# Performance work log

Hardware: AMD Instinct MI355X
Metric: run time of the kernel (lower is better)

The kernel has to match this reference:

```python
import jax, jax.numpy as jnp
import numpy as np

BN_EPS = 1e-5
N_SH, N_SS, N_HH, D = 1195, 390, 805, 64


def _gcn(x, edge_index, W, b, n_nodes, mean):
    # per-edge message = Linear(x_j); lin(x)[src] == lin(x[src])
    h = x @ W + b                                   # [N, out]
    msg = h[edge_index[0]]                          # gather sources -> [E, out]
    agg = jax.ops.segment_sum(msg, edge_index[1], num_segments=n_nodes)
    if mean:
        cnt = jax.ops.segment_sum(jnp.ones((edge_index.shape[1],), x.dtype),
                                  edge_index[1], num_segments=n_nodes)
        agg = agg / jnp.maximum(cnt, 1.0)[:, None]
    return jnp.tanh(agg)


def _bn(x, gamma, beta):
    # BatchNorm1d in training mode: biased batch statistics
    m = jnp.mean(x, axis=0)
    v = jnp.var(x, axis=0)
    return (x - m) * jax.lax.rsqrt(v + BN_EPS) * gamma + beta


def setup_inputs() -> dict:
    key = jax.random.key(0)
    ks = jax.random.split(key, 40)
    f32 = jnp.float32

    def lin(k, din, dout):
        k1, k2 = jax.random.split(k)
        s = 1.0 / np.sqrt(din)
        W = jax.random.uniform(k1, (din, dout), f32, -s, s)
        b = jax.random.uniform(k2, (dout,), f32, -s, s)
        return W, b

    inp = {}
    inp["x_SH"] = jnp.arange(N_SH, dtype=jnp.int64 if jax.config.jax_enable_x64 else jnp.int32)
    inp["edge_index_SH"] = jax.random.randint(ks[0], (2, 1_000_000), 0, N_SH)
    inp["x_SS"] = jnp.arange(N_SS)
    inp["edge_index_SS"] = jax.random.randint(ks[1], (2, 200_000), 0, N_SS)
    inp["x_HH"] = jnp.arange(N_HH)
    inp["edge_index_HH"] = jax.random.randint(ks[2], (2, 200_000), 0, N_HH)
    inp["prescription"] = jax.random.uniform(ks[3], (20000, N_SS), f32)
    inp["kgOneHot"] = jax.random.uniform(ks[4], (N_HH, 27), f32)

    inp["emb"] = jax.random.normal(ks[5], (N_SH, D), f32)
    inp["w_sh1"], inp["b_sh1"] = lin(ks[6], D, D)
    inp["w_sh2"], inp["b_sh2"] = lin(ks[7], D, D)
    inp["w_mlp1"], inp["b_mlp1"] = lin(ks[8], D, 256)
    inp["g_bn1"] = jnp.ones((256,), f32); inp["be_bn1"] = jnp.zeros((256,), f32)
    inp["w_sh1h"], inp["b_sh1h"] = lin(ks[9], D, D)
    inp["w_sh2h"], inp["b_sh2h"] = lin(ks[10], D, D)
    inp["w_mlp1h"], inp["b_mlp1h"] = lin(ks[11], D, 256)
    inp["g_bn1h"] = jnp.ones((256,), f32); inp["be_bn1h"] = jnp.zeros((256,), f32)
    inp["w_ss"], inp["b_ss"] = lin(ks[12], D, 256)
    inp["w_hh"], inp["b_hh"] = lin(ks[13], D + 27, 256)
    inp["w_mlp"], inp["b_mlp"] = lin(ks[14], 256, 256)
    inp["g_si"] = jnp.ones((256,), f32); inp["be_si"] = jnp.zeros((256,), f32)
    return inp


def reference(x_SH, edge_index_SH, x_SS, edge_index_SS, x_HH, edge_index_HH,
              prescription, kgOneHot, emb,
              w_sh1, b_sh1, w_sh2, b_sh2, w_mlp1, b_mlp1, g_bn1, be_bn1,
              w_sh1h, b_sh1h, w_sh2h, b_sh2h, w_mlp1h, b_mlp1h, g_bn1h, be_bn1h,
              w_ss, b_ss, w_hh, b_hh, w_mlp, b_mlp, g_si, be_si):
    # symptom branch on SH graph (mean aggregation)
    x1 = emb[x_SH]                                           # [1195, 64]
    x2 = _gcn(x1, edge_index_SH, w_sh1, b_sh1, N_SH, mean=True)
    x6 = _gcn(x2, edge_index_SH, w_sh2, b_sh2, N_SH, mean=True)
    x9 = (x1 + x2 + x6) / 3.0
    x9 = jnp.tanh(_bn(x9 @ w_mlp1 + b_mlp1, g_bn1, be_bn1))  # [1195, 256]

    # herb branch on SH graph
    x22 = _gcn(x1, edge_index_SH, w_sh1h, b_sh1h, N_SH, mean=True)
    x66 = _gcn(x22, edge_index_SH, w_sh2h, b_sh2h, N_SH, mean=True)
    x99 = (x1 + x22 + x66) / 3.0
    x99 = jnp.tanh(_bn(x99 @ w_mlp1h + b_mlp1h, g_bn1h, be_bn1h))

    # SS graph (add aggregation)
    x_ss1 = _gcn(emb[x_SS], edge_index_SS, w_ss, b_ss, N_SS, mean=False)  # [390, 256]

    # HH graph with KG one-hot features appended
    x_hh0 = jnp.concatenate([emb[x_HH], kgOneHot], axis=-1)  # [805, 91]
    x_hh1 = _gcn(x_hh0, edge_index_HH, w_hh, b_hh, N_HH, mean=False)      # [805, 256]

    es = x9[:N_SS] + x_ss1                                   # [390, 256]
    eh = x99[N_SS:] + x_hh1                                  # [805, 256]

    e_synd = prescription @ es                               # [B, 256]
    pre_sum = jnp.sum(prescription, axis=1, keepdims=True)
    e = e_synd / pre_sum
    e = jax.nn.relu(_bn(e @ w_mlp + b_mlp, g_si, be_si))
    return e @ eh.T                                          # [B, 805]
```

## Files before the change

### kernel.cpp

```cpp
#include <hip/hip_runtime.h>
#include <cstddef>
#include <cstdint>

#define N_SH 1195
#define N_SS 390
#define N_HH 805
#define DIM  64

typedef __bf16 bf16_t;
typedef bf16_t bf16x4v __attribute__((ext_vector_type(4)));
typedef bf16_t bf16x8v __attribute__((ext_vector_type(8)));
typedef float f32x4 __attribute__((ext_vector_type(4)));

__device__ inline ushort f2bf(float f) {
    union { float f; uint32_t u; } c; c.f = f;
    uint32_t u = c.u;
    u += 0x7FFFu + ((u >> 16) & 1u);
    return (ushort)(u >> 16);
}

__device__ inline void xcd_swizzle(int gx, int gy, int& bx, int& by) {
    int nwg = gx * gy;
    int lin = by * gx + bx;
    int q = nwg >> 3, r = nwg & 7;
    int xcd = lin & 7, idx = lin >> 3;
    int nt = (xcd < r ? xcd * (q + 1) : r * (q + 1) + (xcd - r) * q) + idx;
    by = nt / gx; bx = nt % gx;
}

__global__ void build_adj_packed_kernel(const int* __restrict__ ei, int E,
                                        int halfStride, uint32_t* __restrict__ T) {
    int i = blockIdx.x * blockDim.x + threadIdx.x;
    if (i < E) {
        int src = ei[i];
        int dst = ei[E + i];
        atomicAdd(&T[(size_t)dst * halfStride + (src >> 1)], 1u << ((src & 1) * 16));
    }
}

__global__ void rowsum_inv_packed_kernel(const uint32_t* __restrict__ T, int R,
                                         int halfStride, float* __restrict__ inv) {
    int row  = blockIdx.x * (blockDim.x / 64) + (threadIdx.x / 64);
    int lane = threadIdx.x & 63;
    if (row >= R) return;
    const uint32_t* p = T + (size_t)row * halfStride;
    uint32_t s = 0;
    for (int c = lane; c < halfStride; c += 64) {
        uint32_t w = p[c];
        s += (w & 0xFFFFu) + (w >> 16);
    }
    for (int off = 32; off > 0; off >>= 1) s += __shfl_down(s, off);
    if (lane == 0) inv[row] = 1.0f / fmaxf((float)s, 1.0f);
}

__global__ void cvt_unpack_kernel(const uint32_t* __restrict__ T, int R, int C,
                                  int halfStride, ushort* __restrict__ out,
                                  int Rp, int Cp) {
    int i = blockIdx.x * blockDim.x + threadIdx.x;
    if (i >= Rp * Cp) return;
    int r = i / Cp, c = i % Cp;
    float v = 0.f;
    if (r < R && c < C) {
        uint32_t w = T[(size_t)r * halfStride + (c >> 1)];
        v = (float)((w >> ((c & 1) * 16)) & 0xFFFFu);
    }
    out[i] = f2bf(v);
}

#define BM 64
#define BN 64
#define BK 16

__global__ __launch_bounds__(256) void gemm_kernel(
    const float* __restrict__ A, const float* __restrict__ B,
    const float* __restrict__ bias, const float* __restrict__ rowScale,
    float* __restrict__ C, int M, int N, int K, int act)
{
    __shared__ float As[BK][BM + 4];
    __shared__ float Bs[BK][BN];
    const int tid  = threadIdx.x;
    const int row0 = blockIdx.y * BM;
    const int col0 = blockIdx.x * BN;
    const int tr  = (tid >> 4) << 2;
    const int tc  = (tid & 15) << 2;
    const int lar = tid >> 2;
    const int lac = (tid & 3) << 2;
    const int lbr = tid >> 4;
    const int lbc = (tid & 15) << 2;

    float acc[4][4] = {{0.f}};

    for (int k0 = 0; k0 < K; k0 += BK) {
        const int gr = row0 + lar;
        const float* Ap = A + (size_t)gr * K + k0 + lac;
        #pragma unroll
        for (int i = 0; i < 4; ++i) {
            int gk = k0 + lac + i;
            As[lac + i][lar] = (gr < M && gk < K) ? Ap[i] : 0.f;
        }
        const int gk = k0 + lbr;
        const float* Bp = B + (size_t)gk * N + col0 + lbc;
        #pragma unroll
        for (int i = 0; i < 4; ++i) {
            int gc = col0 + lbc + i;
            Bs[lbr][lbc + i] = (gk < K && gc < N) ? Bp[i] : 0.f;
        }
        __syncthreads();
        #pragma unroll
        for (int kk = 0; kk < BK; ++kk) {
            float4 a = *reinterpret_cast<const float4*>(&As[kk][tr]);
            float4 b = *reinterpret_cast<const float4*>(&Bs[kk][tc]);
            acc[0][0] += a.x * b.x; acc[0][1] += a.x * b.y; acc[0][2] += a.x * b.z; acc[0][3] += a.x * b.w;
            acc[1][0] += a.y * b.x; acc[1][1] += a.y * b.y; acc[1][2] += a.y * b.z; acc[1][3] += a.y * b.w;
            acc[2][0] += a.z * b.x; acc[2][1] += a.z * b.y; acc[2][2] += a.z * b.z; acc[2][3] += a.z * b.w;
            acc[3][0] += a.w * b.x; acc[3][1] += a.w * b.y; acc[3][2] += a.w * b.z; acc[3][3] += a.w * b.w;
        }
        __syncthreads();
    }

    #pragma unroll
    for (int i = 0; i < 4; ++i) {
        int gr = row0 + tr + i;
        if (gr >= M) continue;
        float rs = rowScale ? rowScale[gr] : 1.0f;
        #pragma unroll
        for (int j = 0; j < 4; ++j) {
            int gc = col0 + tc + j;
            if (gc >= N) continue;
            float v = acc[i][j];
            if (bias) v += bias[gc];
            v *= rs;
            if (act == 1) v = tanhf(v);
            C[(size_t)gr * N + gc] = v;
        }
    }
}

#define LDT 40

__global__ __launch_bounds__(256) void mfma_gemm_kernel(
    const ushort* __restrict__ A, const ushort* __restrict__ Bt,
    int M, int Nw, int K, int lda,
    const float* __restrict__ bias, const float* __restrict__ rowScale,
    float* __restrict__ outF, ushort* __restrict__ outB, ushort* __restrict__ outLo,
    int ldo, float* __restrict__ statsOut)
{
    __shared__ __align__(16) ushort As[128 * LDT];
    __shared__ __align__(16) ushort Bs[128 * LDT];
    __shared__ float cs[256];
    const int tid  = threadIdx.x;
    int bx = blockIdx.x, by = blockIdx.y;
    xcd_swizzle(gridDim.x, gridDim.y, bx, by);
    const int row0 = by * 128;
    const int col0 = bx * 128;
    const int wid  = tid >> 6, lane = tid & 63;
    const int wr = wid >> 1, wc = wid & 1;
    const int l15 = lane & 15, lg = lane >> 4;
    const int kg = lg * 4;
    const int sr = tid >> 2;
    const int sc = (tid & 3) * 8;

    const ushort* pA0 = A  + (size_t)(row0 + sr)      * lda + sc;
    const ushort* pA1 = A  + (size_t)(row0 + sr + 64) * lda + sc;
    const ushort* pB0 = Bt + (size_t)(col0 + sr)      * lda + sc;
    const ushort* pB1 = Bt + (size_t)(col0 + sr + 64) * lda + sc;

    uint4 ra0 = *reinterpret_cast<const uint4*>(pA0);
    uint4 ra1 = *reinterpret_cast<const uint4*>(pA1);
    uint4 rb0 = *reinterpret_cast<const uint4*>(pB0);
    uint4 rb1 = *reinterpret_cast<const uint4*>(pB1);

    f32x4 acc[4][4];
    #pragma unroll
    for (int m = 0; m < 4; ++m)
        #pragma unroll
        for (int n = 0; n < 4; ++n) acc[m][n] = (f32x4)0.f;

    for (int k0 = 0; k0 < K; k0 += 32) {
        *reinterpret_cast<uint4*>(&As[sr * LDT + sc])        = ra0;
        *reinterpret_cast<uint4*>(&As[(sr + 64) * LDT + sc]) = ra1;
        *reinterpret_cast<uint4*>(&Bs[sr * LDT + sc])        = rb0;
        *reinterpret_cast<uint4*>(&Bs[(sr + 64) * LDT + sc]) = rb1;
        __syncthreads();
        if (k0 + 32 < K) {
            ra0 = *reinterpret_cast<const uint4*>(pA0 + k0 + 32);
            ra1 = *reinterpret_cast<const uint4*>(pA1 + k0 + 32);
            rb0 = *reinterpret_cast<const uint4*>(pB0 + k0 + 32);
            rb1 = *reinterpret_cast<const uint4*>(pB1 + k0 + 32);
        }

        bf16x8v af[4], bfr[4];
        #pragma unroll
        for (int m = 0; m < 4; ++m) {
            int ar = wr * 64 + m * 16 + l15;
            bf16x4v lo = *reinterpret_cast<const bf16x4v*>(&As[ar * LDT + kg]);
            bf16x4v hi = *reinterpret_cast<const bf16x4v*>(&As[ar * LDT + kg + 16]);
            af[m] = __builtin_shufflevector(lo, hi, 0, 1, 2, 3, 4, 5, 6, 7);
        }
        #pragma unroll
        for (int n = 0; n < 4; ++n) {
            int br = wc * 64 + n * 16 + l15;
            bf16x4v lo = *reinterpret_cast<const bf16x4v*>(&Bs[br * LDT + kg]);
            bf16x4v hi = *reinterpret_cast<const bf16x4v*>(&Bs[br * LDT + kg + 16]);
            bfr[n] = __builtin_shufflevector(lo, hi, 0, 1, 2, 3, 4, 5, 6, 7);
        }
        #pragma unroll
        for (int m = 0; m < 4; ++m)
            #pragma unroll
            for (int n = 0; n < 4; ++n)
                acc[m][n] = __builtin_amdgcn_mfma_f32_16x16x32_bf16(af[m], bfr[n], acc[m][n], 0, 0, 0);
        __syncthreads();
    }

    float ls[4] = {0.f, 0.f, 0.f, 0.f}, lq[4] = {0.f, 0.f, 0.f, 0.f};
    #pragma unroll
    for (int m = 0; m < 4; ++m) {
        int grow_base = row0 + wr * 64 + m * 16 + kg;
        #pragma unroll
        for (int j = 0; j < 4; ++j) {
            int grow = grow_base + j;
            if (grow >= M) continue;
            float rs = rowScale ? rowScale[grow] : 1.0f;
            #pragma unroll
            for (int n = 0; n < 4; ++n) {
                int gcol = col0 + wc * 64 + n * 16 + l15;
                if (gcol >= Nw) continue;
                float v = acc[m][n][j];
                if (bias) v += bias[gcol];
                v *= rs;
                if (outB) {
                    ushort h = f2bf(v);
                    outB[(size_t)grow * ldo + gcol] = h;
                    if (outLo) {
                        float hv = __uint_as_float(((uint32_t)h) << 16);
                        outLo[(size_t)grow * ldo + gcol] = f2bf(v - hv);
                    }
                } else {
                    outF[(size_t)grow * ldo + gcol] = v;
                    ls[n] += v; lq[n] += v * v;
                }
            }
        }
    }

    if (statsOut) {
        if (tid < 256) cs[tid] = 0.f;
        __syncthreads();
        #pragma unroll
        for (int n = 0; n < 4; ++n) {
            int lc = wc * 64 + n * 16 + l15;
            atomicAdd(&cs[lc], ls[n]);
            atomicAdd(&cs[128 + lc], lq[n]);
        }
        __syncthreads();
        if (tid < 128) {
            atomicAdd(&statsOut[col0 + tid], cs[tid]);
            atomicAdd(&statsOut[256 + col0 + tid], cs[128 + tid]);
        }
    }
}

__device__ inline void loadP8(const float* __restrict__ rowp, int c0, bool rv,
                              float* a, float& s) {
    if (rv && c0 + 8 <= N_SS) {
        float2 x0 = *reinterpret_cast<const float2*>(rowp + c0);
        float2 x1 = *reinterpret_cast<const float2*>(rowp + c0 + 2);
        float2 x2 = *reinterpret_cast<const float2*>(rowp + c0 + 4);
        float2 x3 = *reinterpret_cast<const float2*>(rowp + c0 + 6);
        a[0] = x0.x; a[1] = x0.y; a[2] = x1.x; a[3] = x1.y;
        a[4] = x2.x; a[5] = x2.y; a[6] = x3.x; a[7] = x3.y;
    } else {
        #pragma unroll
        for (int i = 0; i < 8; ++i) a[i] = (rv && (c0 + i) < N_SS) ? rowp[c0 + i] : 0.f;
    }
    #pragma unroll
    for (int i = 0; i < 8; ++i) s += a[i];
}

__global__ __launch_bounds__(256) void mfma_c1_kernel(
    const float* __restrict__ Pm, const ushort* __restrict__ Bt,
    int M, ushort* __restrict__ outB, ushort* __restrict__ outLo, int ldo)
{
    __shared__ __align__(16) ushort As[128 * LDT];
    __shared__ __align__(16) ushort Bs[128 * LDT];
    __shared__ float sums[128];
    const int tid  = threadIdx.x;
// ... 155 lines not shown
            *reinterpret_cast<uint4*>(&As[sr * LDT + sc]) = *reinterpret_cast<const uint4*>(h);
            h[0] = (bf16_t)fmaxf(a10.x * s8[0] + t8[0], 0.f);
            h[1] = (bf16_t)fmaxf(a10.y * s8[1] + t8[1], 0.f);
            h[2] = (bf16_t)fmaxf(a10.z * s8[2] + t8[2], 0.f);
            h[3] = (bf16_t)fmaxf(a10.w * s8[3] + t8[3], 0.f);
            h[4] = (bf16_t)fmaxf(a11.x * s8[4] + t8[4], 0.f);
            h[5] = (bf16_t)fmaxf(a11.y * s8[5] + t8[5], 0.f);
            h[6] = (bf16_t)fmaxf(a11.z * s8[6] + t8[6], 0.f);
            h[7] = (bf16_t)fmaxf(a11.w * s8[7] + t8[7], 0.f);
            *reinterpret_cast<uint4*>(&As[(sr + 64) * LDT + sc]) = *reinterpret_cast<const uint4*>(h);
        }
        *reinterpret_cast<uint4*>(&Bs[sr * LDT + sc])        = b0;
        *reinterpret_cast<uint4*>(&Bs[(sr + 64) * LDT + sc]) = b1;
        __syncthreads();
        if (k0 + 32 < 256) {
            a00 = *reinterpret_cast<const float4*>(pA0 + k0 + 32);
            a01 = *reinterpret_cast<const float4*>(pA0 + k0 + 36);
            a10 = *reinterpret_cast<const float4*>(pA1 + k0 + 32);
            a11 = *reinterpret_cast<const float4*>(pA1 + k0 + 36);
            b0  = *reinterpret_cast<const uint4*>(pB0 + k0 + 32);
            b1  = *reinterpret_cast<const uint4*>(pB1 + k0 + 32);
        }

        bf16x8v af[4], bfr[4];
        #pragma unroll
        for (int m = 0; m < 4; ++m) {
            int ar = wr * 64 + m * 16 + l15;
            bf16x4v lo = *reinterpret_cast<const bf16x4v*>(&As[ar * LDT + kg]);
            bf16x4v hi = *reinterpret_cast<const bf16x4v*>(&As[ar * LDT + kg + 16]);
            af[m] = __builtin_shufflevector(lo, hi, 0, 1, 2, 3, 4, 5, 6, 7);
        }
        #pragma unroll
        for (int n = 0; n < 4; ++n) {
            int br = wc * 64 + n * 16 + l15;
            bf16x4v lo = *reinterpret_cast<const bf16x4v*>(&Bs[br * LDT + kg]);
            bf16x4v hi = *reinterpret_cast<const bf16x4v*>(&Bs[br * LDT + kg + 16]);
            bfr[n] = __builtin_shufflevector(lo, hi, 0, 1, 2, 3, 4, 5, 6, 7);
        }
        #pragma unroll
        for (int m = 0; m < 4; ++m)
            #pragma unroll
            for (int n = 0; n < 4; ++n)
                acc[m][n] = __builtin_amdgcn_mfma_f32_16x16x32_bf16(af[m], bfr[n], acc[m][n], 0, 0, 0);
        __syncthreads();
    }

    #pragma unroll
    for (int m = 0; m < 4; ++m) {
        int grow_base = row0 + wr * 64 + m * 16 + kg;
        #pragma unroll
        for (int j = 0; j < 4; ++j) {
            int grow = grow_base + j;
            if (grow >= M) continue;
            #pragma unroll
            for (int n = 0; n < 4; ++n) {
                int gcol = col0 + wc * 64 + n * 16 + l15;
                if (gcol >= Nw) continue;
                outF[(size_t)grow * ldo + gcol] = acc[m][n][j];
            }
        }
    }
}

__global__ __launch_bounds__(256) void mfma_splitk_kernel(
    const ushort* __restrict__ A, const ushort* __restrict__ Bt,
    int M, int K, int lda, int kChunk, int Ntot,
    float* __restrict__ part)
{
    __shared__ __align__(16) ushort As[128 * LDT];
    __shared__ __align__(16) ushort Bs[128 * LDT];
    const int tid  = threadIdx.x;
    const int row0 = blockIdx.y * 128;
    const int col0 = blockIdx.x * 128;
    const int wid  = tid >> 6, lane = tid & 63;
    const int wr = wid >> 1, wc = wid & 1;
    const int l15 = lane & 15, lg = lane >> 4;
    const int kg = lg * 4;
    const int sr = tid >> 2;
    const int sc = (tid & 3) * 8;

    const int k0s = blockIdx.z * kChunk;
    const int k0e = (k0s + kChunk < K) ? k0s + kChunk : K;

    const ushort* pA0 = A  + (size_t)(row0 + sr)      * lda + sc;
    const ushort* pA1 = A  + (size_t)(row0 + sr + 64) * lda + sc;
    const ushort* pB0 = Bt + (size_t)(col0 + sr)      * lda + sc;
    const ushort* pB1 = Bt + (size_t)(col0 + sr + 64) * lda + sc;

    uint4 ra0 = *reinterpret_cast<const uint4*>(pA0 + k0s);
    uint4 ra1 = *reinterpret_cast<const uint4*>(pA1 + k0s);
    uint4 rb0 = *reinterpret_cast<const uint4*>(pB0 + k0s);
    uint4 rb1 = *reinterpret_cast<const uint4*>(pB1 + k0s);

    f32x4 acc[4][4];
    #pragma unroll
    for (int m = 0; m < 4; ++m)
        #pragma unroll
        for (int n = 0; n < 4; ++n) acc[m][n] = (f32x4)0.f;

    for (int k0 = k0s; k0 < k0e; k0 += 32) {
        *reinterpret_cast<uint4*>(&As[sr * LDT + sc])        = ra0;
        *reinterpret_cast<uint4*>(&As[(sr + 64) * LDT + sc]) = ra1;
        *reinterpret_cast<uint4*>(&Bs[sr * LDT + sc])        = rb0;
        *reinterpret_cast<uint4*>(&Bs[(sr + 64) * LDT + sc]) = rb1;
        __syncthreads();
        if (k0 + 32 < k0e) {
            ra0 = *reinterpret_cast<const uint4*>(pA0 + k0 + 32);
            ra1 = *reinterpret_cast<const uint4*>(pA1 + k0 + 32);
            rb0 = *reinterpret_cast<const uint4*>(pB0 + k0 + 32);
            rb1 = *reinterpret_cast<const uint4*>(pB1 + k0 + 32);
        }

        bf16x8v af[4], bfr[4];
        #pragma unroll
        for (int m = 0; m < 4; ++m) {
            int ar = wr * 64 + m * 16 + l15;
            bf16x4v lo = *reinterpret_cast<const bf16x4v*>(&As[ar * LDT + kg]);
            bf16x4v hi = *reinterpret_cast<const bf16x4v*>(&As[ar * LDT + kg + 16]);
            af[m] = __builtin_shufflevector(lo, hi, 0, 1, 2, 3, 4, 5, 6, 7);
        }
        #pragma unroll
        for (int n = 0; n < 4; ++n) {
            int br = wc * 64 + n * 16 + l15;
            bf16x4v lo = *reinterpret_cast<const bf16x4v*>(&Bs[br * LDT + kg]);
            bf16x4v hi = *reinterpret_cast<const bf16x4v*>(&Bs[br * LDT + kg + 16]);
            bfr[n] = __builtin_shufflevector(lo, hi, 0, 1, 2, 3, 4, 5, 6, 7);
        }
        #pragma unroll
        for (int m = 0; m < 4; ++m)
            #pragma unroll
            for (int n = 0; n < 4; ++n)
                acc[m][n] = __builtin_amdgcn_mfma_f32_16x16x32_bf16(af[m], bfr[n], acc[m][n], 0, 0, 0);
        __syncthreads();
    }

    float* pslab = part + (size_t)blockIdx.z * M * Ntot;
    #pragma unroll
    for (int m = 0; m < 4; ++m) {
        int grow_base = row0 + wr * 64 + m * 16 + kg;
        #pragma unroll
        for (int j = 0; j < 4; ++j) {
            int grow = grow_base + j;
            if (grow >= M) continue;
            #pragma unroll
            for (int n = 0; n < 4; ++n) {
                int gcol = col0 + wc * 64 + n * 16 + l15;
                pslab[(size_t)grow * Ntot + gcol] = acc[m][n][j];
            }
        }
    }
}

__global__ void reduce_tanh_kernel(const float* __restrict__ part, int S, int M, int N,
                                   const float* __restrict__ rs, float* __restrict__ out) {
    int i = blockIdx.x * blockDim.x + threadIdx.x;
    if (i >= M * N) return;
    int r = i / N;
    float s = 0.f;
    for (int z = 0; z < S; ++z) s += part[(size_t)z * M * N + i];
    if (rs) s *= rs[r];
    out[i] = tanhf(s);
}

__global__ void transpose_cvt_kernel(const float* __restrict__ in, int K, int N, int ldin,
                                     ushort* __restrict__ out, int Kp) {
    int i = blockIdx.x * blockDim.x + threadIdx.x;
    if (i >= N * Kp) return;
    int n = i / Kp, k = i % Kp;
    float v = (k < K) ? in[(size_t)k * ldin + n] : 0.f;
    out[i] = f2bf(v);
}

__global__ void make_cat_weights_kernel(
    const float* __restrict__ w_sh1, const float* __restrict__ w_sh1h,
    const float* __restrict__ b_sh1, const float* __restrict__ b_sh1h,
    const float* __restrict__ w_sh2, const float* __restrict__ w_sh2h,
    const float* __restrict__ b_sh2, const float* __restrict__ b_sh2h,
    const float* __restrict__ w_mlp1, const float* __restrict__ w_mlp1h,
    const float* __restrict__ b_mlp1, const float* __restrict__ b_mlp1h,
    float* __restrict__ W1cat, float* __restrict__ b1cat,
    float* __restrict__ W2bd,  float* __restrict__ b2cat,
    float* __restrict__ WMbd,  float* __restrict__ bMcat)
{
    int i = blockIdx.x * blockDim.x + threadIdx.x;
    if (i < 64 * 128) {
        int k = i >> 7, j = i & 127;
        W1cat[i] = (j < 64) ? w_sh1[k * 64 + j] : w_sh1h[k * 64 + (j - 64)];
        return;
    }
    i -= 64 * 128;
    if (i < 128) { b1cat[i] = (i < 64) ? b_sh1[i] : b_sh1h[i - 64]; return; }
    i -= 128;
    if (i < 128 * 128) {
        int k = i >> 7, j = i & 127;
        float v = 0.f;
        if (k < 64 && j < 64) v = w_sh2[k * 64 + j];
        else if (k >= 64 && j >= 64) v = w_sh2h[(k - 64) * 64 + (j - 64)];
        W2bd[i] = v;
        return;
    }
    i -= 128 * 128;
    if (i < 128) { b2cat[i] = (i < 64) ? b_sh2[i] : b_sh2h[i - 64]; return; }
    i -= 128;
    if (i < 128 * 512) {
        int k = i >> 9, j = i & 511;
        float v = 0.f;
        if (j < 256) { if (k < 64) v = w_mlp1[k * 256 + j]; }
        else         { if (k >= 64) v = w_mlp1h[(k - 64) * 256 + (j - 256)]; }
        WMbd[i] = v;
        return;
    }
    i -= 128 * 512;
    if (i < 512) { bMcat[i] = (i < 256) ? b_mlp1[i] : b_mlp1h[i - 256]; }
}

__global__ void avg3cat_kernel(const float* __restrict__ emb, const float* __restrict__ x2cat,
                               const float* __restrict__ x6cat, float* __restrict__ o) {
    int i = blockIdx.x * blockDim.x + threadIdx.x;
    if (i >= N_SH * 128) return;
    int r = i >> 7, j = i & 127;
    o[i] = (emb[r * 64 + (j & 63)] + x2cat[i] + x6cat[i]) * (1.0f / 3.0f);
}

__global__ void concat_hh_kernel(const float* __restrict__ emb, const float* __restrict__ kg,
                                 float* __restrict__ out) {
    int i = blockIdx.x * blockDim.x + threadIdx.x;
    const int n = N_HH * 91;
    if (i >= n) return;
    int r = i / 91, c = i % 91;
    out[i] = (c < DIM) ? emb[r * DIM + c] : kg[r * 27 + (c - DIM)];
}

__global__ void make_esbt_kernel(const float* __restrict__ x9cat, const float* __restrict__ ss1,
                                 ushort* __restrict__ out, int Kp) {
    int i = blockIdx.x * blockDim.x + threadIdx.x;
    if (i >= 256 * Kp) return;
    int n = i / Kp, k = i % Kp;
    float v = (k < N_SS) ? (x9cat[(size_t)k * 512 + n] + ss1[(size_t)k * 256 + n]) : 0.f;
    out[i] = f2bf(v);
}

__global__ void make_wmlp2_kernel(const float* __restrict__ wm, ushort* __restrict__ out) {
    int i = blockIdx.x * blockDim.x + threadIdx.x;
    if (i >= 256 * 512) return;
    int n = i >> 9, k = i & 511;
    out[i] = f2bf(wm[(size_t)(k & 255) * 256 + n]);
}

__global__ void make_ehb_kernel(const float* __restrict__ x9cat, const float* __restrict__ hh1,
                                ushort* __restrict__ out, int Rp) {
    int i = blockIdx.x * blockDim.x + threadIdx.x;
    if (i >= Rp * 256) return;
    int r = i >> 8, c = i & 255;
    float v = (r < N_HH) ? (x9cat[(size_t)(N_SS + r) * 512 + 256 + c] + hh1[(size_t)r * 256 + c]) : 0.f;
    out[i] = f2bf(v);
}

__global__ void bn_stats_cat_kernel(const float* __restrict__ X, int M,
                                    float* __restrict__ stats) {
    int j = threadIdx.x;
    float s = 0.f, ss = 0.f;
    for (int r = blockIdx.x; r < M; r += gridDim.x) {
        float v = X[(size_t)r * 512 + j];
        s += v; ss += v * v;
    }
    atomicAdd(&stats[j], s);
    atomicAdd(&stats[512 + j], ss);
}

__global__ void bn_apply_cat_kernel(const float* __restrict__ X, const float* __restrict__ stats,
                                    const float* __restrict__ g1, const float* __restrict__ be1,
                                    const float* __restrict__ g2, const float* __restrict__ be2,
                                    int M, float* __restrict__ out) {
    int i = blockIdx.x * blockDim.x + threadIdx.x;
    if (i >= M * 512) return;
    int j = i & 511;
    float invM = 1.0f / (float)M;
    float mean = stats[j] * invM;
    float var  = fmaxf(stats[512 + j] * invM - mean * mean, 0.f);
    float ga = (j < 256) ? g1[j]  : g2[j - 256];
    float bb = (j < 256) ? be1[j] : be2[j - 256];
    float y = (X[i] - mean) * rsqrtf(var + 1e-5f) * ga + bb;
    out[i] = tanhf(y);
}

__global__ void bn_finalize_kernel(const float* __restrict__ stats,
                                   const float* __restrict__ g, const float* __restrict__ be,
                                   int M, float* __restrict__ scale, float* __restrict__ shift) {
    int j = threadIdx.x;
    float invM = 1.0f / (float)M;
    float mean = stats[j] * invM;
    float var  = fmaxf(stats[256 + j] * invM - mean * mean, 0.f);
    float sc = g[j] * rsqrtf(var + 1e-5f);
    scale[j] = sc;
    shift[j] = be[j] - mean * sc;
}

extern "C" void kernel_launch(void* const* d_in, const int* in_sizes, int n_in,
                              void* d_out, int out_size, void* d_ws, size_t ws_size,
                              hipStream_t stream) {
    const int*   eiSH = (const int*)d_in[1];
    const int*   eiSS = (const int*)d_in[3];
    const int*   eiHH = (const int*)d_in[5];
    const float* P    = (const float*)d_in[6];
    const float* kg   = (const float*)d_in[7];
    const float* emb  = (const float*)d_in[8];
    const float* w_sh1  = (const float*)d_in[9];   const float* b_sh1  = (const float*)d_in[10];
    const float* w_sh2  = (const float*)d_in[11];  const float* b_sh2  = (const float*)d_in[12];
    const float* w_mlp1 = (const float*)d_in[13];  const float* b_mlp1 = (const float*)d_in[14];
    const float* g_bn1  = (const float*)d_in[15];  const float* be_bn1 = (const float*)d_in[16];
    const float* w_sh1h = (const float*)d_in[17];  const float* b_sh1h = (const float*)d_in[18];
    const float* w_sh2h = (const float*)d_in[19];  const float* b_sh2h = (const float*)d_in[20];
    const float* w_mlp1h= (const float*)d_in[21];  const float* b_mlp1h= (const float*)d_in[22];
    const float* g_bn1h = (const float*)d_in[23];  const float* be_bn1h= (const float*)d_in[24];
    const float* w_ss   = (const float*)d_in[25];  const float* b_ss   = (const float*)d_in[26];
    const float* w_hh   = (const float*)d_in[27];  const float* b_hh   = (const float*)d_in[28];
    const float* w_mlp  = (const float*)d_in[29];  const float* b_mlp  = (const float*)d_in[30];
    const float* g_si   = (const float*)d_in[31];  const float* be_si  = (const float*)d_in[32];
    float* out = (float*)d_out;

    const int E_SH = in_sizes[1] / 2;
    const int E_SS = in_sizes[3] / 2;
    const int E_HH = in_sizes[5] / 2;
    const int B    = in_sizes[6] / N_SS;
    const int Mp   = ((B + 127) / 128) * 128;
    const int KP1  = 416;
    const int NP3  = 896;
    const int KSH  = 1216;
    const int KHH  = 832;
    const int HS_SH = (N_SH + 1) / 2;
    const int HS_SS = (N_SS + 1) / 2;
    const int HS_HH = (N_HH + 1) / 2;

    float* w = (float*)d_ws;
    size_t off = 0;
    auto alloc = [&](size_t n) { float* p = w + off; off += (n + 3) & ~(size_t)3; return p; };

    float* cntInv  = alloc(N_SH);
    float* stats   = alloc(1024);
    float* bnScale = alloc(256);
    float* bnShift = alloc(256);
    float* W1cat   = alloc(64 * 128);
    float* b1cat   = alloc(128);
    float* W2bd    = alloc(128 * 128);
    float* b2cat   = alloc(128);
    float* WMbd    = alloc(128 * 512);
    float* bMcat   = alloc(512);
    ushort* adjb   = (ushort*)alloc((size_t)1280 * KSH / 2);
    ushort* adjSSb = (ushort*)alloc((size_t)512 * KP1 / 2);
    ushort* adjHHb = (ushort*)alloc((size_t)896 * KHH / 2);
    float* tmpL    = alloc((size_t)N_SH * 128);
    ushort* HT     = (ushort*)alloc((size_t)128 * KSH / 2);
    float* x2cat   = alloc((size_t)N_SH * 128);
    float* x6cat   = alloc((size_t)N_SH * 128);
    float* x9a2    = alloc((size_t)N_SH * 128);
    float* tmpBN   = alloc((size_t)N_SH * 512);
    float* x9cat   = alloc((size_t)N_SH * 512);
    float* ss1     = alloc((size_t)N_SS * 256);
    float* hh1     = alloc((size_t)N_HH * 256);
    float* xhh0    = alloc((size_t)N_HH * 91);
    ushort* HSST   = (ushort*)alloc((size_t)256 * KP1 / 2);
    ushort* HHHT   = (ushort*)alloc((size_t)256 * KHH / 2);
    ushort* es_bT  = (ushort*)alloc((size_t)256 * KP1 / 2);
    ushort* wmlp2  = (ushort*)alloc((size_t)256 * 512 / 2);
    ushort* eh_b   = (ushort*)alloc((size_t)NP3 * 256 / 2);
    float* regionA = alloc((size_t)Mp * 256);
    uint32_t* uSH  = (uint32_t*)regionA;
    uint32_t* uSS  = uSH + (size_t)N_SH * HS_SH;
    uint32_t* uHH  = uSS + (size_t)N_SS * HS_SS;
    size_t packed_words = (size_t)N_SH * HS_SH + (size_t)N_SS * HS_SS + (size_t)N_HH * HS_HH;
    float*  bufM   = regionA;
    float* regionB = alloc((size_t)Mp * 256);
    float*  partials = regionB;
    ushort* e_hilo = (ushort*)regionB;
    (void)ws_size; (void)n_in; (void)out_size;

    auto gemm = [&](const float* Am, const float* Bm, const float* bias, const float* rs,
                    float* C, int M, int N, int K, int act) {
        dim3 g((N + BN - 1) / BN, (M + BM - 1) / BM);
        gemm_kernel<<<g, 256, 0, stream>>>(Am, Bm, bias, rs, C, M, N, K, act);
    };
    auto mgemm = [&](const ushort* Am, const ushort* Bm, int M, int Np, int Nw, int K, int lda,
                     const float* bias, const float* rs,
                     float* oF, ushort* oB, ushort* oLo, int ldo, float* st) {
        dim3 g(Np / 128, (M + 127) / 128);
        mfma_gemm_kernel<<<g, 256, 0, stream>>>(Am, Bm, M, Nw, K, lda, bias, rs, oF, oB, oLo, ldo, st);
    };
    auto splitk = [&](const ushort* Am, const ushort* Bm, int M, int Mtiles, int K, int lda,
                      int Ntot, int S, const float* rs, float* outp) {
        dim3 g(Ntot / 128, Mtiles, S);
        mfma_splitk_kernel<<<g, 256, 0, stream>>>(Am, Bm, M, K, lda, 128, Ntot, partials);
        reduce_tanh_kernel<<<(M * Ntot + 255) / 256, 256, 0, stream>>>(partials, S, M, Ntot, rs, outp);
    };

    hipMemsetAsync(uSH, 0, packed_words * sizeof(uint32_t), stream);
    build_adj_packed_kernel<<<(E_SH + 255) / 256, 256, 0, stream>>>(eiSH, E_SH, HS_SH, uSH);
    build_adj_packed_kernel<<<(E_SS + 255) / 256, 256, 0, stream>>>(eiSS, E_SS, HS_SS, uSS);
    build_adj_packed_kernel<<<(E_HH + 255) / 256, 256, 0, stream>>>(eiHH, E_HH, HS_HH, uHH);
    rowsum_inv_packed_kernel<<<(N_SH + 3) / 4, 256, 0, stream>>>(uSH, N_SH, HS_SH, cntInv);
    cvt_unpack_kernel<<<(1280 * KSH + 255) / 256, 256, 0, stream>>>(uSH, N_SH, N_SH, HS_SH, adjb, 1280, KSH);
    cvt_unpack_kernel<<<(512 * KP1 + 255) / 256, 256, 0, stream>>>(uSS, N_SS, N_SS, HS_SS, adjSSb, 512, KP1);
    cvt_unpack_kernel<<<(896 * KHH + 255) / 256, 256, 0, stream>>>(uHH, N_HH, N_HH, HS_HH, adjHHb, 896, KHH);

    make_cat_weights_kernel<<<(90880 + 255) / 256, 256, 0, stream>>>(
        w_sh1, w_sh1h, b_sh1, b_sh1h, w_sh2, w_sh2h, b_sh2, b_sh2h,
        w_mlp1, w_mlp1h, b_mlp1, b_mlp1h,
        W1cat, b1cat, W2bd, b2cat, WMbd, bMcat);

    gemm(emb, W1cat, b1cat, nullptr, tmpL, N_SH, 128, 64, 0);
    transpose_cvt_kernel<<<(128 * KSH + 255) / 256, 256, 0, stream>>>(tmpL, N_SH, 128, 128, HT, KSH);
    splitk(adjb, HT, N_SH, 10, KSH, KSH, 128, 10, cntInv, x2cat);
    gemm(x2cat, W2bd, b2cat, nullptr, tmpL, N_SH, 128, 128, 0);
    transpose_cvt_kernel<<<(128 * KSH + 255) / 256, 256, 0, stream>>>(tmpL, N_SH, 128, 128, HT, KSH);
    splitk(adjb, HT, N_SH, 10, KSH, KSH, 128, 10, cntInv, x6cat);
    avg3cat_kernel<<<(N_SH * 128 + 255) / 256, 256, 0, stream>>>(emb, x2cat, x6cat, x9a2);
    gemm(x9a2, WMbd, bMcat, nullptr, tmpBN, N_SH, 512, 128, 0);
    hipMemsetAsync(stats, 0, 1024 * sizeof(float), stream);
    bn_stats_cat_kernel<<<64, 512, 0, stream>>>(tmpBN, N_SH, stats);
    bn_apply_cat_kernel<<<(N_SH * 512 + 255) / 256, 256, 0, stream>>>(
        tmpBN, stats, g_bn1, be_bn1, g_bn1h, be_bn1h, N_SH, x9cat);

    gemm(emb, w_ss, b_ss, nullptr, tmpBN, N_SS, 256, 64, 0);
    transpose_cvt_kernel<<<(256 * KP1 + 255) / 256, 256, 0, stream>>>(tmpBN, N_SS, 256, 256, HSST, KP1);
    splitk(adjSSb, HSST, N_SS, 4, KP1, KP1, 256, 4, nullptr, ss1);

    concat_hh_kernel<<<(N_HH * 91 + 255) / 256, 256, 0, stream>>>(emb, kg, xhh0);
    gemm(xhh0, w_hh, b_hh, nullptr, tmpBN, N_HH, 256, 91, 0);
    transpose_cvt_kernel<<<(256 * KHH + 255) / 256, 256, 0, stream>>>(tmpBN, N_HH, 256, 256, HHHT, KHH);
    splitk(adjHHb, HHHT, N_HH, 7, KHH, KHH, 256, 7, nullptr, hh1);

    make_esbt_kernel<<<(256 * KP1 + 255) / 256, 256, 0, stream>>>(x9cat, ss1, es_bT, KP1);
    make_wmlp2_kernel<<<(256 * 512 + 255) / 256, 256, 0, stream>>>(w_mlp, wmlp2);
    make_ehb_kernel<<<(NP3 * 256 + 255) / 256, 256, 0, stream>>>(x9cat, hh1, eh_b, NP3);
    hipMemsetAsync(stats, 0, 512 * sizeof(float), stream);

    {
        dim3 g(2, (B + 127) / 128);
        mfma_c1_kernel<<<g, 256, 0, stream>>>(P, es_bT, B, e_hilo, e_hilo + 256, 512);
    }
    mgemm(e_hilo, wmlp2, B, 256, 256, 512, 512, b_mlp, nullptr,
          bufM, nullptr, nullptr, 256, stats);
    bn_finalize_kernel<<<1, 256, 0, stream>>>(stats, g_si, be_si, B, bnScale, bnShift);
    {
        dim3 g(NP3 / 128, (B + 127) / 128);
        mfma_c3_kernel<<<g, 256, 0, stream>>>(bufM, eh_b, B, N_HH, bnScale, bnShift, out, N_HH);
    }
}
```

Baseline: 342.4 us.

## Fuse small prep kernels and fold transposes and BN stats into GEMM epilogues

Merges the three adjacency-build kernels and the three unpack kernels into single launches. The fp32 GEMM epilogue now writes transposed bf16 output directly, which removes the transpose_cvt passes, and it also accumulates BN column statistics, which removes bn_stats_cat. The avg3 step is folded into the reduce_tanh epilogue, wmlp2 construction moves into make_cat_weights, and several memsets become one contiguous memset. The aim is fewer launches and fewer intermediate round trips through memory, at the cost of strided transposed stores and more shared-memory atomics in the GEMM epilogue.

```diff
diff --git a/kernel.cpp b/kernel.cpp
--- a/kernel.cpp
+++ b/kernel.cpp
@@ -28,13 +28,23 @@
     by = nt / gx; bx = nt % gx;
 }
 
-__global__ void build_adj_packed_kernel(const int* __restrict__ ei, int E,
-                                        int halfStride, uint32_t* __restrict__ T) {
+__global__ void build_adj3_kernel(
+    const int* __restrict__ e1, int E1, int hs1, uint32_t* __restrict__ T1,
+    const int* __restrict__ e2, int E2, int hs2, uint32_t* __restrict__ T2,
+    const int* __restrict__ e3, int E3, int hs3, uint32_t* __restrict__ T3)
+{
     int i = blockIdx.x * blockDim.x + threadIdx.x;
-    if (i < E) {
-        int src = ei[i];
-        int dst = ei[E + i];
-        atomicAdd(&T[(size_t)dst * halfStride + (src >> 1)], 1u << ((src & 1) * 16));
+    if (i < E1) {
+        int src = e1[i], dst = e1[E1 + i];
+        atomicAdd(&T1[(size_t)dst * hs1 + (src >> 1)], 1u << ((src & 1) * 16));
+    } else if (i < E1 + E2) {
+        int j = i - E1;
+        int src = e2[j], dst = e2[E2 + j];
+        atomicAdd(&T2[(size_t)dst * hs2 + (src >> 1)], 1u << ((src & 1) * 16));
+    } else if (i < E1 + E2 + E3) {
+        int j = i - E1 - E2;
+        int src = e3[j], dst = e3[E3 + j];
+        atomicAdd(&T3[(size_t)dst * hs3 + (src >> 1)], 1u << ((src & 1) * 16));
     }
 }
 
@@ -53,18 +63,28 @@
     if (lane == 0) inv[row] = 1.0f / fmaxf((float)s, 1.0f);
 }
 
-__global__ void cvt_unpack_kernel(const uint32_t* __restrict__ T, int R, int C,
-                                  int halfStride, ushort* __restrict__ out,
-                                  int Rp, int Cp) {
-    int i = blockIdx.x * blockDim.x + threadIdx.x;
-    if (i >= Rp * Cp) return;
+__device__ inline void unpack_one(const uint32_t* __restrict__ T, int R, int C,
+                                  int hs, ushort* __restrict__ out, int Cp, int i) {
     int r = i / Cp, c = i % Cp;
     float v = 0.f;
     if (r < R && c < C) {
-        uint32_t w = T[(size_t)r * halfStride + (c >> 1)];
+        uint32_t w = T[(size_t)r * hs + (c >> 1)];
         v = (float)((w >> ((c & 1) * 16)) & 0xFFFFu);
     }
     out[i] = f2bf(v);
+}
+
+__global__ void cvt_unpack3_kernel(
+    const uint32_t* __restrict__ T1, int hs1, ushort* __restrict__ o1, int n1, int Cp1,
+    const uint32_t* __restrict__ T2, int hs2, ushort* __restrict__ o2, int n2, int Cp2,
+    const uint32_t* __restrict__ T3, int hs3, ushort* __restrict__ o3, int n3, int Cp3)
+{
+    int i = blockIdx.x * blockDim.x + threadIdx.x;
+    if (i < n1) { unpack_one(T1, N_SH, N_SH, hs1, o1, Cp1, i); return; }
+    i -= n1;
+    if (i < n2) { unpack_one(T2, N_SS, N_SS, hs2, o2, Cp2, i); return; }
+    i -= n2;
+    if (i < n3) { unpack_one(T3, N_HH, N_HH, hs3, o3, Cp3, i); }
 }
 
 #define BM 64
@@ -73,11 +93,13 @@
 
 __global__ __launch_bounds__(256) void gemm_kernel(
     const float* __restrict__ A, const float* __restrict__ B,
-    const float* __restrict__ bias, const float* __restrict__ rowScale,
-    float* __restrict__ C, int M, int N, int K, int act)
+    const float* __restrict__ bias,
+    float* __restrict__ C, ushort* __restrict__ outT, int ldt,
+    int M, int N, int K, float* __restrict__ statsOut, int statsStride)
 {
     __shared__ float As[BK][BM + 4];
     __shared__ float Bs[BK][BN];
+    __shared__ float cs[128];
     const int tid  = threadIdx.x;
     const int row0 = blockIdx.y * BM;
     const int col0 = blockIdx.x * BN;
@@ -118,20 +140,35 @@
         __syncthreads();
     }
 
+    float ls[4] = {0.f, 0.f, 0.f, 0.f}, lq[4] = {0.f, 0.f, 0.f, 0.f};
     #pragma unroll
     for (int i = 0; i < 4; ++i) {
         int gr = row0 + tr + i;
         if (gr >= M) continue;
-        float rs = rowScale ? rowScale[gr] : 1.0f;
         #pragma unroll
         for (int j = 0; j < 4; ++j) {
             int gc = col0 + tc + j;
             if (gc >= N) continue;
             float v = acc[i][j];
             if (bias) v += bias[gc];
-            v *= rs;
-            if (act == 1) v = tanhf(v);
-            C[(size_t)gr * N + gc] = v;
+            if (outT) outT[(size_t)gc * ldt + gr] = f2bf(v);
+            else      C[(size_t)gr * N + gc] = v;
+            ls[j] += v; lq[j] += v * v;
+        }
+    }
+
+    if (statsOut) {
+        if (tid < 128) cs[tid] = 0.f;
+        __syncthreads();
+        #pragma unroll
+        for (int j = 0; j < 4; ++j) {
+            atomicAdd(&cs[tc + j], ls[j]);
+            atomicAdd(&cs[64 + tc + j], lq[j]);
+        }
+        __syncthreads();
+        if (tid < 64) {
+            atomicAdd(&statsOut[col0 + tid], cs[tid]);
+            atomicAdd(&statsOut[statsStride + col0 + tid], cs[64 + tid]);
         }
     }
 }
@@ -593,23 +630,19 @@
 }
 
 __global__ void reduce_tanh_kernel(const float* __restrict__ part, int S, int M, int N,
-                                   const float* __restrict__ rs, float* __restrict__ out) {
+                                   const float* __restrict__ rs,
+                                   const float* __restrict__ emb,
+                                   const float* __restrict__ prev,
+                                   float* __restrict__ out) {
     int i = blockIdx.x * blockDim.x + threadIdx.x;
     if (i >= M * N) return;
-    int r = i / N;
+    int r = i / N, j = i - r * N;
     float s = 0.f;
     for (int z = 0; z < S; ++z) s += part[(size_t)z * M * N + i];
     if (rs) s *= rs[r];
-    out[i] = tanhf(s);
-}
-
-__global__ void transpose_cvt_kernel(const float* __restrict__ in, int K, int N, int ldin,
-                                     ushort* __restrict__ out, int Kp) {
-    int i = blockIdx.x * blockDim.x + threadIdx.x;
-    if (i >= N * Kp) return;
-    int n = i / Kp, k = i % Kp;
-    float v = (k < K) ? in[(size_t)k * ldin + n] : 0.f;
-    out[i] = f2bf(v);
+    float t = tanhf(s);
+    if (emb) out[i] = (emb[r * 64 + (j & 63)] + prev[i] + t) * (1.0f / 3.0f);
+    else     out[i] = t;
 }
 
 __global__ void make_cat_weights_kernel(
@@ -619,9 +652,11 @@
     const float* __restrict__ b_sh2, const float* __restrict__ b_sh2h,
     const float* __restrict__ w_mlp1, const float* __restrict__ w_mlp1h,
     const float* __restrict__ b_mlp1, const float* __restrict__ b_mlp1h,
+    const float* __restrict__ w_mlp,
     float* __restrict__ W1cat, float* __restrict__ b1cat,
     float* __restrict__ W2bd,  float* __restrict__ b2cat,
-    float* __restrict__ WMbd,  float* __restrict__ bMcat)
+    float* __restrict__ WMbd,  float* __restrict__ bMcat,
+    ushort* __restrict__ wmlp2)
 {
     int i = blockIdx.x * blockDim.x + threadIdx.x;
     if (i < 64 * 128) {
@@ -652,15 +687,12 @@
         return;
     }
     i -= 128 * 512;
-    if (i < 512) { bMcat[i] = (i < 256) ? b_mlp1[i] : b_mlp1h[i - 256]; }
-}
-
-__global__ void avg3cat_kernel(const float* __restrict__ emb, const float* __restrict__ x2cat,
-                               const float* __restrict__ x6cat, float* __restrict__ o) {
-    int i = blockIdx.x * blockDim.x + threadIdx.x;
-    if (i >= N_SH * 128) return;
-    int r = i >> 7, j = i & 127;
-    o[i] = (emb[r * 64 + (j & 63)] + x2cat[i] + x6cat[i]) * (1.0f / 3.0f);
+    if (i < 512) { bMcat[i] = (i < 256) ? b_mlp1[i] : b_mlp1h[i - 256]; return; }
+    i -= 512;
+    if (i < 256 * 512) {
+        int n = i >> 9, k = i & 511;
+        wmlp2[i] = f2bf(w_mlp[(size_t)(k & 255) * 256 + n]);
+    }
 }
 
 __global__ void concat_hh_kernel(const float* __restrict__ emb, const float* __restrict__ kg,
@@ -681,13 +713,6 @@
     out[i] = f2bf(v);
 }
 
-__global__ void make_wmlp2_kernel(const float* __restrict__ wm, ushort* __restrict__ out) {
-    int i = blockIdx.x * blockDim.x + threadIdx.x;
-    if (i >= 256 * 512) return;
-    int n = i >> 9, k = i & 511;
-    out[i] = f2bf(wm[(size_t)(k & 255) * 256 + n]);
-}
-
 __global__ void make_ehb_kernel(const float* __restrict__ x9cat, const float* __restrict__ hh1,
                                 ushort* __restrict__ out, int Rp) {
     int i = blockIdx.x * blockDim.x + threadIdx.x;
@@ -695,18 +720,6 @@
     int r = i >> 8, c = i & 255;
     float v = (r < N_HH) ? (x9cat[(size_t)(N_SS + r) * 512 + 256 + c] + hh1[(size_t)r * 256 + c]) : 0.f;
     out[i] = f2bf(v);
-}
-
-__global__ void bn_stats_cat_kernel(const float* __restrict__ X, int M,
-                                    float* __restrict__ stats) {
-    int j = threadIdx.x;
-    float s = 0.f, ss = 0.f;
-    for (int r = blockIdx.x; r < M; r += gridDim.x) {
-        float v = X[(size_t)r * 512 + j];
-        s += v; ss += v * v;
-    }
-    atomicAdd(&stats[j], s);
-    atomicAdd(&stats[512 + j], ss);
 }
 
 __global__ void bn_apply_cat_kernel(const float* __restrict__ X, const float* __restrict__ stats,
@@ -777,8 +790,13 @@
     size_t off = 0;
     auto alloc = [&](size_t n) { float* p = w + off; off += (n + 3) & ~(size_t)3; return p; };
 
-    float* cntInv  = alloc(N_SH);
-    float* stats   = alloc(1024);
+    float* cntInv   = alloc(N_SH);
+    float* statsCat = alloc(1024);
+    float* statsC2  = alloc(512);
+    ushort* HT      = (ushort*)alloc((size_t)128 * KSH / 2);
+    ushort* HSST    = (ushort*)alloc((size_t)256 * KP1 / 2);
+    ushort* HHHT    = (ushort*)alloc((size_t)256 * KHH / 2);
+    float* zeroEnd  = w + off;
     float* bnScale = alloc(256);
     float* bnShift = alloc(256);
     float* W1cat   = alloc(64 * 128);
@@ -787,23 +805,18 @@
     float* b2cat   = alloc(128);
     float* WMbd    = alloc(128 * 512);
     float* bMcat   = alloc(512);
+    ushort* wmlp2  = (ushort*)alloc((size_t)256 * 512 / 2);
     ushort* adjb   = (ushort*)alloc((size_t)1280 * KSH / 2);
     ushort* adjSSb = (ushort*)alloc((size_t)512 * KP1 / 2);
     ushort* adjHHb = (ushort*)alloc((size_t)896 * KHH / 2);
-    float* tmpL    = alloc((size_t)N_SH * 128);
-    ushort* HT     = (ushort*)alloc((size_t)128 * KSH / 2);
     float* x2cat   = alloc((size_t)N_SH * 128);
-    float* x6cat   = alloc((size_t)N_SH * 128);
     float* x9a2    = alloc((size_t)N_SH * 128);
     float* tmpBN   = alloc((size_t)N_SH * 512);
     float* x9cat   = alloc((size_t)N_SH * 512);
     float* ss1     = alloc((size_t)N_SS * 256);
     float* hh1     = alloc((size_t)N_HH * 256);
     float* xhh0    = alloc((size_t)N_HH * 91);
-    ushort* HSST   = (ushort*)alloc((size_t)256 * KP1 / 2);
-    ushort* HHHT   = (ushort*)alloc((size_t)256 * KHH / 2);
     ushort* es_bT  = (ushort*)alloc((size_t)256 * KP1 / 2);
-    ushort* wmlp2  = (ushort*)alloc((size_t)256 * 512 / 2);
     ushort* eh_b   = (ushort*)alloc((size_t)NP3 * 256 / 2);
     float* regionA = alloc((size_t)Mp * 256);
     uint32_t* uSH  = (uint32_t*)regionA;
@@ -816,72 +829,74 @@
     ushort* e_hilo = (ushort*)regionB;
     (void)ws_size; (void)n_in; (void)out_size;
 
-    auto gemm = [&](const float* Am, const float* Bm, const float* bias, const float* rs,
-                    float* C, int M, int N, int K, int act) {
+    auto gemmT = [&](const float* Am, const float* Bm, const float* bias,
+                     ushort* oT, int ldt, int M, int N, int K) {
         dim3 g((N + BN - 1) / BN, (M + BM - 1) / BM);
-        gemm_kernel<<<g, 256, 0, stream>>>(Am, Bm, bias, rs, C, M, N, K, act);
+        gemm_kernel<<<g, 256, 0, stream>>>(Am, Bm, bias, nullptr, oT, ldt, M, N, K, nullptr, 0);
     };
-    auto mgemm = [&](const ushort* Am, const ushort* Bm, int M, int Np, int Nw, int K, int lda,
-                     const float* bias, const float* rs,
-                     float* oF, ushort* oB, ushort* oLo, int ldo, float* st) {
-        dim3 g(Np / 128, (M + 127) / 128);
-        mfma_gemm_kernel<<<g, 256, 0, stream>>>(Am, Bm, M, Nw, K, lda, bias, rs, oF, oB, oLo, ldo, st);
+    auto gemmF = [&](const float* Am, const float* Bm, const float* bias,
+                     float* C, int M, int N, int K, float* st, int sstride) {
+        dim3 g((N + BN - 1) / BN, (M + BM - 1) / BM);
+        gemm_kernel<<<g, 256, 0, stream>>>(Am, Bm, bias, C, nullptr, 0, M, N, K, st, sstride);
     };
     auto splitk = [&](const ushort* Am, const ushort* Bm, int M, int Mtiles, int K, int lda,
-                      int Ntot, int S, const float* rs, float* outp) {
+                      int Ntot, int S, const float* rs, const float* embA, const float* prev,
+                      float* outp) {
         dim3 g(Ntot / 128, Mtiles, S);
         mfma_splitk_kernel<<<g, 256, 0, stream>>>(Am, Bm, M, K, lda, 128, Ntot, partials);
-        reduce_tanh_kernel<<<(M * Ntot + 255) / 256, 256, 0, stream>>>(partials, S, M, Ntot, rs, outp);
+        reduce_tanh_kernel<<<(M * Ntot + 255) / 256, 256, 0, stream>>>(
+            partials, S, M, Ntot, rs, embA, prev, outp);
     };
 
     hipMemsetAsync(uSH, 0, packed_words * sizeof(uint32_t), stream);
-    build_adj_packed_kernel<<<(E_SH + 255) / 256, 256, 0, stream>>>(eiSH, E_SH, HS_SH, uSH);
-    build_adj_packed_kernel<<<(E_SS + 255) / 256, 256, 0, stream>>>(eiSS, E_SS, HS_SS, uSS);
-    build_adj_packed_kernel<<<(E_HH + 255) / 256, 256, 0, stream>>>(eiHH, E_HH, HS_HH, uHH);
+    hipMemsetAsync(statsCat, 0, (size_t)((char*)zeroEnd - (char*)statsCat), stream);
+
+    {
+        int Etot = E_SH + E_SS + E_HH;
+        build_adj3_kernel<<<(Etot + 255) / 256, 256, 0, stream>>>(
+            eiSH, E_SH, HS_SH, uSH, eiSS, E_SS, HS_SS, uSS, eiHH, E_HH, HS_HH, uHH);
+    }
     rowsum_inv_packed_kernel<<<(N_SH + 3) / 4, 256, 0, stream>>>(uSH, N_SH, HS_SH, cntInv);
-    cvt_unpack_kernel<<<(1280 * KSH + 255) / 256, 256, 0, stream>>>(uSH, N_SH, N_SH, HS_SH, adjb, 1280, KSH);
-    cvt_unpack_kernel<<<(512 * KP1 + 255) / 256, 256, 0, stream>>>(uSS, N_SS, N_SS, HS_SS, adjSSb, 512, KP1);
-    cvt_unpack_kernel<<<(896 * KHH + 255) / 256, 256, 0, stream>>>(uHH, N_HH, N_HH, HS_HH, adjHHb, 896, KHH);
-
-    make_cat_weights_kernel<<<(90880 + 255) / 256, 256, 0, stream>>>(
+    {
+        int n1 = 1280 * KSH, n2 = 512 * KP1, n3 = 896 * KHH;
+        cvt_unpack3_kernel<<<(n1 + n2 + n3 + 255) / 256, 256, 0, stream>>>(
+            uSH, HS_SH, adjb, n1, KSH, uSS, HS_SS, adjSSb, n2, KP1, uHH, HS_HH, adjHHb, n3, KHH);
+    }
+
+    make_cat_weights_kernel<<<(90880 + 131072 + 255) / 256, 256, 0, stream>>>(
         w_sh1, w_sh1h, b_sh1, b_sh1h, w_sh2, w_sh2h, b_sh2, b_sh2h,
-        w_mlp1, w_mlp1h, b_mlp1, b_mlp1h,
-        W1cat, b1cat, W2bd, b2cat, WMbd, bMcat);
-
-    gemm(emb, W1cat, b1cat, nullptr, tmpL, N_SH, 128, 64, 0);
-    transpose_cvt_kernel<<<(128 * KSH + 255) / 256, 256, 0, stream>>>(tmpL, N_SH, 128, 128, HT, KSH);
-    splitk(adjb, HT, N_SH, 10, KSH, KSH, 128, 10, cntInv, x2cat);
-    gemm(x2cat, W2bd, b2cat, nullptr, tmpL, N_SH, 128, 128, 0);
-    transpose_cvt_kernel<<<(128 * KSH + 255) / 256, 256, 0, stream>>>(tmpL, N_SH, 128, 128, HT, KSH);
-    splitk(adjb, HT, N_SH, 10, KSH, KSH, 128, 10, cntInv, x6cat);
-    avg3cat_kernel<<<(N_SH * 128 + 255) / 256, 256, 0, stream>>>(emb, x2cat, x6cat, x9a2);
-    gemm(x9a2, WMbd, bMcat, nullptr, tmpBN, N_SH, 512, 128, 0);
-    hipMemsetAsync(stats, 0, 1024 * sizeof(float), stream);
-    bn_stats_cat_kernel<<<64, 512, 0, stream>>>(tmpBN, N_SH, stats);
+        w_mlp1, w_mlp1h, b_mlp1, b_mlp1h, w_mlp,
+        W1cat, b1cat, W2bd, b2cat, WMbd, bMcat, wmlp2);
+
+    gemmT(emb, W1cat, b1cat, HT, KSH, N_SH, 128, 64);
+    splitk(adjb, HT, N_SH, 10, KSH, KSH, 128, 10, cntInv, nullptr, nullptr, x2cat);
+    gemmT(x2cat, W2bd, b2cat, HT, KSH, N_SH, 128, 128);
+    splitk(adjb, HT, N_SH, 10, KSH, KSH, 128, 10, cntInv, emb, x2cat, x9a2);
+    gemmF(x9a2, WMbd, bMcat, tmpBN, N_SH, 512, 128, statsCat, 512);
     bn_apply_cat_kernel<<<(N_SH * 512 + 255) / 256, 256, 0, stream>>>(
-        tmpBN, stats, g_bn1, be_bn1, g_bn1h, be_bn1h, N_SH, x9cat);
-
-    gemm(emb, w_ss, b_ss, nullptr, tmpBN, N_SS, 256, 64, 0);
-    transpose_cvt_kernel<<<(256 * KP1 + 255) / 256, 256, 0, stream>>>(tmpBN, N_SS, 256, 256, HSST, KP1);
-    splitk(adjSSb, HSST, N_SS, 4, KP1, KP1, 256, 4, nullptr, ss1);
+        tmpBN, statsCat, g_bn1, be_bn1, g_bn1h, be_bn1h, N_SH, x9cat);
+
+    gemmT(emb, w_ss, b_ss, HSST, KP1, N_SS, 256, 64);
+    splitk(adjSSb, HSST, N_SS, 4, KP1, KP1, 256, 4, nullptr, nullptr, nullptr, ss1);
 
     concat_hh_kernel<<<(N_HH * 91 + 255) / 256, 256, 0, stream>>>(emb, kg, xhh0);
-    gemm(xhh0, w_hh, b_hh, nullptr, tmpBN, N_HH, 256, 91, 0);
-    transpose_cvt_kernel<<<(256 * KHH + 255) / 256, 256, 0, stream>>>(tmpBN, N_HH, 256, 256, HHHT, KHH);
-    splitk(adjHHb, HHHT, N_HH, 7, KHH, KHH, 256, 7, nullptr, hh1);
+    gemmT(xhh0, w_hh, b_hh, HHHT, KHH, N_HH, 256, 91);
+    splitk(adjHHb, HHHT, N_HH, 7, KHH, KHH, 256, 7, nullptr, nullptr, nullptr, hh1);
 
     make_esbt_kernel<<<(256 * KP1 + 255) / 256, 256, 0, stream>>>(x9cat, ss1, es_bT, KP1);
-    make_wmlp2_kernel<<<(256 * 512 + 255) / 256, 256, 0, stream>>>(w_mlp, wmlp2);
     make_ehb_kernel<<<(NP3 * 256 + 255) / 256, 256, 0, stream>>>(x9cat, hh1, eh_b, NP3);
-    hipMemsetAsync(stats, 0, 512 * sizeof(float), stream);
 
     {
         dim3 g(2, (B + 127) / 128);
         mfma_c1_kernel<<<g, 256, 0, stream>>>(P, es_bT, B, e_hilo, e_hilo + 256, 512);
     }
-    mgemm(e_hilo, wmlp2, B, 256, 256, 512, 512, b_mlp, nullptr,
-          bufM, nullptr, nullptr, 256, stats);
-    bn_finalize_kernel<<<1, 256, 0, stream>>>(stats, g_si, be_si, B, bnScale, bnShift);
+    {
+        dim3 g(2, (B + 127) / 128);
+        mfma_gemm_kernel<<<g, 256, 0, stream>>>(e_hilo, wmlp2, B, 256, 512, 512,
+                                                b_mlp, nullptr, bufM, nullptr, nullptr, 256,
+                                                statsC2);
+    }
+    bn_finalize_kernel<<<1, 256, 0, stream>>>(statsC2, g_si, be_si, B, bnScale, bnShift);
     {
         dim3 g(NP3 / 128, (B + 127) / 128);
         mfma_c3_kernel<<<g, 256, 0, stream>>>(bufM, eh_b, B, N_HH, bnScale, bnShift, out, N_HH);
```

After: 318.0 us. 1.08x faster.
